# Optimization experiments

Hardware: AMD Instinct MI355X
Metric: run time of the kernel (lower is better)

The kernel has to match this reference:

```python
import math
import jax, jax.numpy as jnp
import numpy as np

B, S, D, H = 4, 1024, 1024, 16
DK = D // H
NEG = jnp.float32(-1e32)
EPS = 1e-5


def setup_inputs() -> dict:
    key = jax.random.key(0)
    ks = jax.random.split(key, 10)
    s = 1.0 / math.sqrt(D)
    return {
        "query": jax.random.normal(ks[0], (B, S, D), jnp.float32),
        "key": jax.random.normal(ks[1], (B, S, D), jnp.float32),
        "values": jax.random.normal(ks[2], (B, S, D), jnp.float32),
        "lens": jax.random.randint(ks[3], (B,), 0, S).astype(jnp.int32),
        "state_weight": jax.random.normal(ks[4], (1, H, S, S), jnp.float32),
        # params (kq_same=True -> k shares q_linear weights)
        "Wq": jax.random.normal(ks[5], (D, D), jnp.float32) * s,
        "bq": jnp.zeros((D,), jnp.float32),
        "Wv": jax.random.normal(ks[6], (D, D), jnp.float32) * s,
        "bv": jnp.zeros((D,), jnp.float32),
        "Wo": jax.random.normal(ks[7], (D, D), jnp.float32) * s,
        "bo": jnp.zeros((D,), jnp.float32),
        "gamma": jnp.ones((D,), jnp.float32),
        "beta": jnp.zeros((D,), jnp.float32),
    }


def reference(query, key, values, lens, state_weight, Wq, bq, Wv, bv, Wo, bo, gamma, beta):
    # eval-mode forward of DTransformerLayer (peek_cur=False -> strictly causal)
    b, s, d = query.shape
    mask = jnp.tril(jnp.ones((s, s), bool), -1)[None, None]  # [1,1,S,S]

    q = (query @ Wq + bq).reshape(b, s, H, DK).transpose(0, 2, 1, 3)   # bhsd
    k = (key @ Wq + bq).reshape(b, s, H, DK).transpose(0, 2, 1, 3)     # shared weights (kq_same)
    v = (values @ Wv + bv).reshape(b, s, H, DK).transpose(0, 2, 1, 3)

    scores = jnp.einsum('bhqd,bhkd->bhqk', q, k) / math.sqrt(DK)
    scores = jnp.where(mask, scores, NEG)
    scores = jnp.where(mask, scores + state_weight, NEG)
    attn = jax.nn.softmax(scores, axis=-1)
    attn = jnp.where(mask, attn, 0.0)  # fully-masked rows (row 0) -> zeros, matching torch

    ctx = jnp.einsum('bhqk,bhkd->bhqd', attn, v).transpose(0, 2, 1, 3).reshape(b, s, d)
    out = ctx @ Wo + bo

    x = query + out  # dropout is identity in eval
    mu = jnp.mean(x, axis=-1, keepdims=True)
    var = jnp.mean(jnp.square(x - mu), axis=-1, keepdims=True)
    return (x - mu) * jax.lax.rsqrt(var + EPS) * gamma + beta
```

## Files before the change

kernel.cpp:

```cpp
#include <hip/hip_runtime.h>

#define B_ 4
#define S_ 1024
#define D_ 1024
#define H_ 16
#define DK_ 64

typedef __attribute__((ext_vector_type(8))) short short8;
typedef __attribute__((ext_vector_type(4))) float f32x4;
typedef __attribute__((ext_vector_type(16))) float f32x16;

static __device__ __forceinline__ unsigned bf16rne(float x) {
    unsigned b = __float_as_uint(x);
    return (b + 0x7FFFu + ((b >> 16) & 1u)) >> 16;
}

__global__ __launch_bounds__(256) void cvt3_bf16(
    const float* __restrict__ q, const float* __restrict__ k,
    const float* __restrict__ v, ushort* __restrict__ out)
{
    const size_t i = ((size_t)blockIdx.x * 256 + threadIdx.x) * 8;
    const size_t FM = (size_t)4 * 1024 * 1024;
    const float* in = (i < FM) ? q : (i < 2 * FM) ? k : v;
    const size_t off = i & (FM - 1);
    const float4 a = *reinterpret_cast<const float4*>(in + off);
    const float4 b = *reinterpret_cast<const float4*>(in + off + 4);
    union { ushort u[8]; int4 vv; } p;
    p.u[0] = (ushort)bf16rne(a.x); p.u[1] = (ushort)bf16rne(a.y);
    p.u[2] = (ushort)bf16rne(a.z); p.u[3] = (ushort)bf16rne(a.w);
    p.u[4] = (ushort)bf16rne(b.x); p.u[5] = (ushort)bf16rne(b.y);
    p.u[6] = (ushort)bf16rne(b.z); p.u[7] = (ushort)bf16rne(b.w);
    *reinterpret_cast<int4*>(out + i) = p.vv;
}

__global__ __launch_bounds__(256) void transpose_cvt3(
    const float* __restrict__ W0, const float* __restrict__ W1,
    const float* __restrict__ W2, ushort* __restrict__ T0,
    ushort* __restrict__ T1, ushort* __restrict__ T2)
{
    __shared__ float ts[32][33];
    const float* W = (blockIdx.z == 0) ? W0 : (blockIdx.z == 1) ? W1 : W2;
    ushort*     Wt = (blockIdx.z == 0) ? T0 : (blockIdx.z == 1) ? T1 : T2;
    const int t  = threadIdx.x;
    const int k0 = blockIdx.y * 32, n0 = blockIdx.x * 32;
    const int r  = t >> 3, c4 = (t & 7) * 4;
    const float4 v = *reinterpret_cast<const float4*>(&W[(size_t)(k0 + r) * 1024 + n0 + c4]);
    ts[r][c4] = v.x; ts[r][c4 + 1] = v.y; ts[r][c4 + 2] = v.z; ts[r][c4 + 3] = v.w;
    __syncthreads();
    ushort4 o;
    o.x = (ushort)bf16rne(ts[c4    ][r]);
    o.y = (ushort)bf16rne(ts[c4 + 1][r]);
    o.z = (ushort)bf16rne(ts[c4 + 2][r]);
    o.w = (ushort)bf16rne(ts[c4 + 3][r]);
    *reinterpret_cast<ushort4*>(&Wt[(size_t)(n0 + r) * 1024 + k0 + c4]) = o;
}

template<int MODE>
__global__ __launch_bounds__(256) void gemm_mfma(
    const ushort* __restrict__ X, const ushort* __restrict__ Wt,
    const float* __restrict__ bias, const float* __restrict__ resid,
    void* __restrict__ out0, void* __restrict__ out1)
{
    __shared__ ushort As[64 * 64];
    __shared__ ushort Bs[128 * 64];

    const int t    = threadIdx.x;
    const int lane = t & 63;
    const int w    = t >> 6;

    const int cpx     = gridDim.x >> 3;
    const int logical = (blockIdx.x & 7) * cpx + (blockIdx.x >> 3);
    const int bm = logical >> 3;
    const int bn = logical & 7;

    const int srow   = lane >> 3;
    const int schunk = (lane & 7) ^ srow;
    const ushort* ag[2];
    const ushort* bg[4];
#pragma unroll
    for (int j = 0; j < 2; ++j)
        ag[j] = X  + (size_t)(bm * 64 + (j * 4 + w) * 8 + srow) * 1024 + schunk * 8;
#pragma unroll
    for (int j = 0; j < 4; ++j)
        bg[j] = Wt + (size_t)(bn * 128 + (j * 4 + w) * 8 + srow) * 1024 + schunk * 8;

#define STAGE(k0)                                                                \
    do {                                                                         \
        _Pragma("unroll")                                                        \
        for (int j = 0; j < 2; ++j)                                              \
            __builtin_amdgcn_global_load_lds(                                    \
                (__attribute__((address_space(1))) const void*)(ag[j] + (k0)),   \
                (__attribute__((address_space(3))) void*)&As[(j * 4 + w) * 512], \
                16, 0, 0);                                                       \
        _Pragma("unroll")                                                        \
        for (int j = 0; j < 4; ++j)                                              \
            __builtin_amdgcn_global_load_lds(                                    \
                (__attribute__((address_space(1))) const void*)(bg[j] + (k0)),   \
                (__attribute__((address_space(3))) void*)&Bs[(j * 4 + w) * 512], \
                16, 0, 0);                                                       \
    } while (0)

    const int fr = lane & 15;
    const int fk = lane >> 4;
    const int wm = w >> 1, wn = w & 1;

    f32x4 acc[2][4];
#pragma unroll
    for (int m = 0; m < 2; ++m)
#pragma unroll
        for (int n = 0; n < 4; ++n) acc[m][n] = (f32x4){0.f, 0.f, 0.f, 0.f};

#pragma unroll 1
    for (int kt = 0; kt < 16; ++kt) {
        STAGE(kt * 64);
        __syncthreads();
#pragma unroll
        for (int ks = 0; ks < 2; ++ks) {
            short8 af[2], bf[4];
#pragma unroll
            for (int m = 0; m < 2; ++m) {
                const int row = wm * 32 + m * 16 + fr;
                af[m] = *reinterpret_cast<const short8*>(
                    &As[row * 64 + (((ks * 4 + fk) ^ (row & 7)) * 8)]);
            }
#pragma unroll
            for (int n = 0; n < 4; ++n) {
                const int row = wn * 64 + n * 16 + fr;
                bf[n] = *reinterpret_cast<const short8*>(
                    &Bs[row * 64 + (((ks * 4 + fk) ^ (row & 7)) * 8)]);
            }
#pragma unroll
            for (int m = 0; m < 2; ++m)
#pragma unroll
                for (int n = 0; n < 4; ++n)
                    acc[m][n] = __builtin_amdgcn_mfma_f32_16x16x32_bf16(
                        af[m], bf[n], acc[m][n], 0, 0, 0);
        }
        __syncthreads();
    }
#undef STAGE

#pragma unroll
    for (int m = 0; m < 2; ++m) {
        const int row0 = bm * 64 + wm * 32 + m * 16 + fk * 4;
#pragma unroll
        for (int n = 0; n < 4; ++n) {
            const int col = bn * 128 + wn * 64 + n * 16 + fr;
            const float bc = bias[col];
            if (MODE == 0) {
                float* o = (float*)out0;
#pragma unroll
                for (int j = 0; j < 4; ++j) {
                    const int row = row0 + j;
                    o[(size_t)row * 1024 + col] =
                        acc[m][n][j] + bc + resid[(size_t)row * 1024 + col];
                }
            } else if (MODE == 1) {
                ushort* o = (row0 < 4096) ? (ushort*)out0 : (ushort*)out1;
                const int r0 = row0 & 4095;
                const int b_ = r0 >> 10, s0 = r0 & 1023;
                const int h  = col >> 6,  dk = col & 63;
#pragma unroll
                for (int j = 0; j < 4; ++j)
                    o[(((size_t)b_ * H_ + h) * S_ + s0 + j) * DK_ + dk] =
                        (ushort)bf16rne(acc[m][n][j] + bc);
            } else {
                ushort* o = (ushort*)out0;
                const int b_ = row0 >> 10, s0 = row0 & 1023;
                const int h  = col >> 6,   dk = col & 63;
                ushort4 pk;
                pk.x = (ushort)bf16rne(acc[m][n][0] + bc);
                pk.y = (ushort)bf16rne(acc[m][n][1] + bc);
                pk.z = (ushort)bf16rne(acc[m][n][2] + bc);
                pk.w = (ushort)bf16rne(acc[m][n][3] + bc);
                *reinterpret_cast<ushort4*>(
                    &o[(((size_t)b_ * H_ + h) * DK_ + dk) * S_ + s0]) = pk;
            }
        }
    }
}

__global__ __launch_bounds__(256) void attn_mfma(
    const ushort* __restrict__ Qh, const ushort* __restrict__ Kh,
    const ushort* __restrict__ Vt, const float* __restrict__ SW,
    ushort* __restrict__ ctx)
{
    __shared__ ushort Ks[2][64 * 64];
    __shared__ ushort Vs[2][64 * 64];

    const int t    = threadIdx.x;
    const int lane = t & 63;
    const int w    = t >> 6;
    const int bid  = blockIdx.x;
    const int bh   = bid & 63;
    const int b    = bh >> 4;
    const int h    = bh & 15;
    int qb = bid >> 6;
    qb = (qb < 4) ? qb : 11 - qb;

    const int ql = lane & 31;
    const int hi = lane >> 5;
    const int qrow  = qb * 128 + ql * 4 + w;
    const int maxt  = 2 * qb + 2;

    const ushort* Kg  = Kh + (size_t)bh * S_ * DK_;
    const ushort* Vg  = Vt + (size_t)bh * DK_ * S_;
    const float*  swp = SW + ((size_t)h * S_ + qrow) * S_;

    const int srow   = lane >> 3;
    const int schunk = (lane & 7) ^ srow;
    const ushort* kg[2];
    const ushort* vg[2];
#pragma unroll
    for (int j = 0; j < 2; ++j) {
        kg[j] = Kg + (size_t)((j * 4 + w) * 8 + srow) * DK_ + schunk * 8;
        vg[j] = Vg + (size_t)((j * 4 + w) * 8 + srow) * S_  + schunk * 8;
    }

#define ASTAGE(buf, k0)                                                          \
    do {                                                                         \
        _Pragma("unroll")                                                        \
        for (int j = 0; j < 2; ++j) {                                            \
            __builtin_amdgcn_global_load_lds(                                    \
                (__attribute__((address_space(1))) const void*)(kg[j] + (size_t)(k0) * DK_), \
                (__attribute__((address_space(3))) void*)&Ks[buf][(j * 4 + w) * 512], \
                16, 0, 0);                                                       \
            __builtin_amdgcn_global_load_lds(                                    \
                (__attribute__((address_space(1))) const void*)(vg[j] + (k0)),   \
                (__attribute__((address_space(3))) void*)&Vs[buf][(j * 4 + w) * 512], \
                16, 0, 0);                                                       \
        }                                                                        \
    } while (0)

    short8 qf[4];
    {
        const ushort* Qg = Qh + ((size_t)bh * S_ + qrow) * DK_;
#pragma unroll
        for (int c = 0; c < 4; ++c) {
            union { int4 i; short8 s; } u;
            u.i = *reinterpret_cast<const int4*>(&Qg[c * 16 + hi * 8]);
            qf[c] = u.s;
        }
    }

    f32x16 accA, accB;
#pragma unroll
    for (int r = 0; r < 16; ++r) { accA[r] = 0.f; accB[r] = 0.f; }
    float mrow = -1e30f, lrow = 0.f;

    ASTAGE(0, 0);

#pragma unroll 1
    for (int kt = 0; kt < maxt; ++kt) {
        const int cur = kt & 1;
        const int k0  = kt * 64;
        if (kt + 1 < maxt) {
            ASTAGE(cur ^ 1, (kt + 1) * 64);
            asm volatile("s_waitcnt vmcnt(4)" ::: "memory");
        } else {
            asm volatile("s_waitcnt vmcnt(0)" ::: "memory");
        }
        __builtin_amdgcn_s_barrier();
        __builtin_amdgcn_sched_barrier(0);

        f32x16 sc[2];
#pragma unroll
        for (int g = 0; g < 2; ++g) {
#pragma unroll
            for (int r = 0; r < 16; ++r) sc[g][r] = 0.f;
            const int row = g * 32 + ql;
#pragma unroll
            for (int c = 0; c < 4; ++c) {
                union { int2 p[2]; short8 s; } u;
                const int ch = ((c * 2 + hi) ^ (row & 7)) * 8;
                u.p[0] = *reinterpret_cast<const int2*>(&Ks[cur][row * 64 + ch]);
                u.p[1] = *reinterpret_cast<const int2*>(&Ks[cur][row * 64 + ch + 4]);
                sc[g] = __builtin_amdgcn_mfma_f32_32x32x16_bf16(u.s, qf[c], sc[g], 0, 0, 0);
            }
        }

        float swv[2][16];
#pragma unroll
        for (int g = 0; g < 2; ++g)
#pragma unroll
            for (int j = 0; j < 4; ++j) {
                const float4 v = *reinterpret_cast<const float4*>(
                    &swp[k0 + g * 32 + hi * 4 + j * 8]);
                swv[g][j * 4 + 0] = v.x; swv[g][j * 4 + 1] = v.y;
                swv[g][j * 4 + 2] = v.z; swv[g][j * 4 + 3] = v.w;
            }

        float p[2][16];
        float tmax = -1e30f;
#pragma unroll
        for (int g = 0; g < 2; ++g)
#pragma unroll
            for (int r = 0; r < 16; ++r) {
                const int key = k0 + g * 32 + (r & 3) + ((r >> 2) << 3) + (hi << 2);
                const float s = (key < qrow) ? sc[g][r] * 0.125f + swv[g][r] : -1e30f;
                p[g][r] = s;
                tmax = fmaxf(tmax, s);
            }
        tmax = fmaxf(tmax, __shfl_xor(tmax, 32, 64));
        const float mnew = fmaxf(mrow, tmax);
        const float corr = __expf(mrow - mnew);
        float psum = 0.f;
#pragma unroll
        for (int g = 0; g < 2; ++g)
#pragma unroll
            for (int r = 0; r < 16; ++r) {
                const float e = (p[g][r] > -1e29f) ? __expf(p[g][r] - mnew) : 0.f;
                p[g][r] = e;
                psum += e;
            }
        psum += __shfl_xor(psum, 32, 64);
        lrow = lrow * corr + psum;
        mrow = mnew;
#pragma unroll
        for (int r = 0; r < 16; ++r) { accA[r] *= corr; accB[r] *= corr; }

        short8 paf[4];
#pragma unroll
        for (int g = 0; g < 2; ++g) {
            unsigned pk[8];
#pragma unroll
            for (int j = 0; j < 8; ++j)
                pk[j] = bf16rne(p[g][2 * j]) | (bf16rne(p[g][2 * j + 1]) << 16);
            unsigned x0 = (unsigned)__shfl_xor((int)pk[0], 32, 64);
            unsigned x1 = (unsigned)__shfl_xor((int)pk[1], 32, 64);
            unsigned x2 = (unsigned)__shfl_xor((int)pk[2], 32, 64);
            unsigned x3 = (unsigned)__shfl_xor((int)pk[3], 32, 64);
            unsigned x4 = (unsigned)__shfl_xor((int)pk[4], 32, 64);
            unsigned x5 = (unsigned)__shfl_xor((int)pk[5], 32, 64);
            unsigned x6 = (unsigned)__shfl_xor((int)pk[6], 32, 64);
            unsigned x7 = (unsigned)__shfl_xor((int)pk[7], 32, 64);
            union { unsigned u[4]; short8 s; } a0, a1;
            a0.u[0] = hi ? x2 : pk[0];
            a0.u[1] = hi ? x3 : pk[1];
            a0.u[2] = hi ? pk[2] : x0;
            a0.u[3] = hi ? pk[3] : x1;
            a1.u[0] = hi ? x6 : pk[4];
            a1.u[1] = hi ? x7 : pk[5];
            a1.u[2] = hi ? pk[6] : x4;
            a1.u[3] = hi ? pk[7] : x5;
            paf[g * 2 + 0] = a0.s;
            paf[g * 2 + 1] = a1.s;
        }

#pragma unroll
        for (int cc = 0; cc < 4; ++cc) {
            const int rowA = ql, rowB = ql + 32;
            const int chA = ((cc * 2 + hi) ^ (rowA & 7)) * 8;
            union { int2 pp[2]; short8 s; } va, vb;
            va.pp[0] = *reinterpret_cast<const int2*>(&Vs[cur][rowA * 64 + chA]);
            va.pp[1] = *reinterpret_cast<const int2*>(&Vs[cur][rowA * 64 + chA + 4]);
            vb.pp[0] = *reinterpret_cast<const int2*>(&Vs[cur][rowB * 64 + chA]);
            vb.pp[1] = *reinterpret_cast<const int2*>(&Vs[cur][rowB * 64 + chA + 4]);
            accA = __builtin_amdgcn_mfma_f32_32x32x16_bf16(va.s, paf[cc], accA, 0, 0, 0);
            accB = __builtin_amdgcn_mfma_f32_32x32x16_bf16(vb.s, paf[cc], accB, 0, 0, 0);
        }

        __builtin_amdgcn_sched_barrier(0);
        __builtin_amdgcn_s_barrier();
        __builtin_amdgcn_sched_barrier(0);
    }
#undef ASTAGE

    const float inv = (lrow > 0.f) ? 1.f / lrow : 0.f;
    ushort* crow_ = ctx + ((size_t)b * S_ + qrow) * D_ + h * DK_;
#pragma unroll
    for (int g = 0; g < 4; ++g) {
        ushort4 oA, oB;
        oA.x = (ushort)bf16rne(accA[4 * g + 0] * inv);
        oA.y = (ushort)bf16rne(accA[4 * g + 1] * inv);
        oA.z = (ushort)bf16rne(accA[4 * g + 2] * inv);
        oA.w = (ushort)bf16rne(accA[4 * g + 3] * inv);
        oB.x = (ushort)bf16rne(accB[4 * g + 0] * inv);
        oB.y = (ushort)bf16rne(accB[4 * g + 1] * inv);
        oB.z = (ushort)bf16rne(accB[4 * g + 2] * inv);
        oB.w = (ushort)bf16rne(accB[4 * g + 3] * inv);
        *reinterpret_cast<ushort4*>(&crow_[g * 8 + hi * 4])      = oA;
        *reinterpret_cast<ushort4*>(&crow_[g * 8 + hi * 4 + 32]) = oB;
    }
}

__global__ __launch_bounds__(256) void layernorm_k(
    const float* __restrict__ x, const float* __restrict__ gamma,
    const float* __restrict__ beta, float* __restrict__ out)
{
    const int row = blockIdx.x;
    const int t   = threadIdx.x;
    const float4 v = *reinterpret_cast<const float4*>(&x[(size_t)row * D_ + (t << 2)]);
    float sum = v.x + v.y + v.z + v.w;
    float sq  = v.x * v.x + v.y * v.y + v.z * v.z + v.w * v.w;
#pragma unroll
    for (int w = 1; w < 64; w <<= 1) {
        sum += __shfl_xor(sum, w, 64);
        sq  += __shfl_xor(sq,  w, 64);
    }
    __shared__ float red[8];
    const int wid = t >> 6;
    if ((t & 63) == 0) { red[wid] = sum; red[wid + 4] = sq; }
    __syncthreads();
    sum = red[0] + red[1] + red[2] + red[3];
    sq  = red[4] + red[5] + red[6] + red[7];
    const float mu  = sum * (1.f / 1024.f);
    const float var = sq * (1.f / 1024.f) - mu * mu;
    const float rs  = rsqrtf(var + 1e-5f);
    const float4 gm = *reinterpret_cast<const float4*>(&gamma[t << 2]);
    const float4 bt = *reinterpret_cast<const float4*>(&beta[t << 2]);
    float4 o;
    o.x = (v.x - mu) * rs * gm.x + bt.x;
    o.y = (v.y - mu) * rs * gm.y + bt.y;
    o.z = (v.z - mu) * rs * gm.z + bt.z;
    o.w = (v.w - mu) * rs * gm.w + bt.w;
    *reinterpret_cast<float4*>(&out[(size_t)row * D_ + (t << 2)]) = o;
}

extern "C" void kernel_launch(void* const* d_in, const int* in_sizes, int n_in,
                              void* d_out, int out_size, void* d_ws, size_t ws_size,
                              hipStream_t stream)
{
    const float* query  = (const float*)d_in[0];
    const float* key    = (const float*)d_in[1];
    const float* values = (const float*)d_in[2];
    const float* SW     = (const float*)d_in[4];
    const float* Wq     = (const float*)d_in[5];
    const float* bq     = (const float*)d_in[6];
    const float* Wv     = (const float*)d_in[7];
    const float* bv     = (const float*)d_in[8];
    const float* Wo     = (const float*)d_in[9];
    const float* bo     = (const float*)d_in[10];
    const float* gamma  = (const float*)d_in[11];
    const float* beta   = (const float*)d_in[12];

    char* ws = (char*)d_ws;
    const size_t MB = 1024 * 1024;
    ushort* qbf = (ushort*)(ws);
    ushort* kbf = (ushort*)(ws +  8 * MB);
    ushort* vbf = (ushort*)(ws + 16 * MB);
    ushort* Wqt = (ushort*)(ws + 24 * MB);
    ushort* Wvt = (ushort*)(ws + 26 * MB);
    ushort* Wot = (ushort*)(ws + 28 * MB);
    ushort* Qh  = (ushort*)(ws + 30 * MB);
    ushort* Kh  = (ushort*)(ws + 38 * MB);
    ushort* Vt  = (ushort*)(ws + 46 * MB);
    ushort* ctxb = qbf;
    float*  xbf  = (float*)(ws + 8 * MB);

    const dim3 blk(256);

    cvt3_bf16<<<dim3(6144), blk, 0, stream>>>(query, key, values, qbf);
    transpose_cvt3<<<dim3(32, 32, 3), blk, 0, stream>>>(Wq, Wv, Wo, Wqt, Wvt, Wot);

    gemm_mfma<1><<<dim3(1024), blk, 0, stream>>>(qbf, Wqt, bq, nullptr, Qh, Kh);
    gemm_mfma<2><<<dim3(512),  blk, 0, stream>>>(vbf, Wvt, bv, nullptr, Vt, nullptr);

    attn_mfma<<<dim3(512), blk, 0, stream>>>(Qh, Kh, Vt, SW, ctxb);

    gemm_mfma<0><<<dim3(512), blk, 0, stream>>>(ctxb, Wot, bo, query, xbf, nullptr);

    layernorm_k<<<dim3(4096), blk, 0, stream>>>(xbf, gamma, beta, (float*)d_out);
}
```

Measured before the change: 139.6 us.

## Split attention key range into two partitions with flash-decoding style merge

Each query block's key tiles are split into two halves, each processed by its own workgroup, doubling the attention grid to 1024 blocks. Partial contexts are written in bf16 along with per-row running max and sum, and a new merge kernel combines them with softmax rescaling. The K/V tiles in shared memory are also relaid out so each lane reads a contiguous 16-byte fragment instead of two swizzled 8-byte reads. This adds an extra kernel launch, extra global traffic for the partials, and an extra bf16 rounding step in exchange for better CU occupancy across the causal workload.

```diff
diff --git a/kernel.cpp b/kernel.cpp
--- a/kernel.cpp
+++ b/kernel.cpp
@@ -183,10 +183,10 @@
 __global__ __launch_bounds__(256) void attn_mfma(
     const ushort* __restrict__ Qh, const ushort* __restrict__ Kh,
     const ushort* __restrict__ Vt, const float* __restrict__ SW,
-    ushort* __restrict__ ctx)
-{
-    __shared__ ushort Ks[2][64 * 64];
-    __shared__ ushort Vs[2][64 * 64];
+    ushort* __restrict__ ctxP, float2* __restrict__ ml)
+{
+    __shared__ ushort Ks[2][4096];
+    __shared__ ushort Vs[2][4096];
 
     const int t    = threadIdx.x;
     const int lane = t & 63;
@@ -195,39 +195,43 @@
     const int bh   = bid & 63;
     const int b    = bh >> 4;
     const int h    = bh & 15;
-    int qb = bid >> 6;
+    const int qp   = bid >> 6;
+    const int p    = qp >> 3;
+    int qb = qp & 7;
     qb = (qb < 4) ? qb : 11 - qb;
 
     const int ql = lane & 31;
     const int hi = lane >> 5;
-    const int qrow  = qb * 128 + ql * 4 + w;
-    const int maxt  = 2 * qb + 2;
+    const int qrow = qb * 128 + ql * 4 + w;
+    const int t0 = p * (qb + 1);
+    const int nt = qb + 1;
 
     const ushort* Kg  = Kh + (size_t)bh * S_ * DK_;
     const ushort* Vg  = Vt + (size_t)bh * DK_ * S_;
     const float*  swp = SW + ((size_t)h * S_ + qrow) * S_;
 
-    const int srow   = lane >> 3;
-    const int schunk = (lane & 7) ^ srow;
-    const ushort* kg[2];
-    const ushort* vg[2];
+    const ushort* kgp[2];
+    const ushort* vgp[2];
 #pragma unroll
     for (int j = 0; j < 2; ++j) {
-        kg[j] = Kg + (size_t)((j * 4 + w) * 8 + srow) * DK_ + schunk * 8;
-        vg[j] = Vg + (size_t)((j * 4 + w) * 8 + srow) * S_  + schunk * 8;
+        const int bb = w * 2 + j;
+        const int g = bb >> 2, c = bb & 3;
+        kgp[j] = Kg + (size_t)(g * 32 + ql) * DK_ + c * 16 + hi * 8;
+        vgp[j] = Vg + (size_t)(g * 32 + ql) * S_  + c * 16 + hi * 8;
     }
 
 #define ASTAGE(buf, k0)                                                          \
     do {                                                                         \
         _Pragma("unroll")                                                        \
         for (int j = 0; j < 2; ++j) {                                            \
+            const int bb = w * 2 + j;                                            \
             __builtin_amdgcn_global_load_lds(                                    \
-                (__attribute__((address_space(1))) const void*)(kg[j] + (size_t)(k0) * DK_), \
-                (__attribute__((address_space(3))) void*)&Ks[buf][(j * 4 + w) * 512], \
+                (__attribute__((address_space(1))) const void*)(kgp[j] + (size_t)(k0) * DK_), \
+                (__attribute__((address_space(3))) void*)&Ks[buf][bb * 512],     \
                 16, 0, 0);                                                       \
             __builtin_amdgcn_global_load_lds(                                    \
-                (__attribute__((address_space(1))) const void*)(vg[j] + (k0)),   \
-                (__attribute__((address_space(3))) void*)&Vs[buf][(j * 4 + w) * 512], \
+                (__attribute__((address_space(1))) const void*)(vgp[j] + (k0)),  \
+                (__attribute__((address_space(3))) void*)&Vs[buf][bb * 512],     \
                 16, 0, 0);                                                       \
         }                                                                        \
     } while (0)
@@ -248,14 +252,14 @@
     for (int r = 0; r < 16; ++r) { accA[r] = 0.f; accB[r] = 0.f; }
     float mrow = -1e30f, lrow = 0.f;
 
-    ASTAGE(0, 0);
+    ASTAGE(0, t0 * 64);
 
 #pragma unroll 1
-    for (int kt = 0; kt < maxt; ++kt) {
+    for (int kt = 0; kt < nt; ++kt) {
         const int cur = kt & 1;
-        const int k0  = kt * 64;
-        if (kt + 1 < maxt) {
-            ASTAGE(cur ^ 1, (kt + 1) * 64);
+        const int k0  = (t0 + kt) * 64;
+        if (kt + 1 < nt) {
+            ASTAGE(cur ^ 1, (t0 + kt + 1) * 64);
             asm volatile("s_waitcnt vmcnt(4)" ::: "memory");
         } else {
             asm volatile("s_waitcnt vmcnt(0)" ::: "memory");
@@ -268,14 +272,11 @@
         for (int g = 0; g < 2; ++g) {
 #pragma unroll
             for (int r = 0; r < 16; ++r) sc[g][r] = 0.f;
-            const int row = g * 32 + ql;
 #pragma unroll
             for (int c = 0; c < 4; ++c) {
-                union { int2 p[2]; short8 s; } u;
-                const int ch = ((c * 2 + hi) ^ (row & 7)) * 8;
-                u.p[0] = *reinterpret_cast<const int2*>(&Ks[cur][row * 64 + ch]);
-                u.p[1] = *reinterpret_cast<const int2*>(&Ks[cur][row * 64 + ch + 4]);
-                sc[g] = __builtin_amdgcn_mfma_f32_32x32x16_bf16(u.s, qf[c], sc[g], 0, 0, 0);
+                const short8 kf = *reinterpret_cast<const short8*>(
+                    &Ks[cur][((g * 4 + c) * 64 + lane) * 8]);
+                sc[g] = __builtin_amdgcn_mfma_f32_32x32x16_bf16(kf, qf[c], sc[g], 0, 0, 0);
             }
         }
 
@@ -290,7 +291,7 @@
                 swv[g][j * 4 + 2] = v.z; swv[g][j * 4 + 3] = v.w;
             }
 
-        float p[2][16];
+        float pr[2][16];
         float tmax = -1e30f;
 #pragma unroll
         for (int g = 0; g < 2; ++g)
@@ -298,7 +299,7 @@
             for (int r = 0; r < 16; ++r) {
                 const int key = k0 + g * 32 + (r & 3) + ((r >> 2) << 3) + (hi << 2);
                 const float s = (key < qrow) ? sc[g][r] * 0.125f + swv[g][r] : -1e30f;
-                p[g][r] = s;
+                pr[g][r] = s;
                 tmax = fmaxf(tmax, s);
             }
         tmax = fmaxf(tmax, __shfl_xor(tmax, 32, 64));
@@ -309,8 +310,8 @@
         for (int g = 0; g < 2; ++g)
 #pragma unroll
             for (int r = 0; r < 16; ++r) {
-                const float e = (p[g][r] > -1e29f) ? __expf(p[g][r] - mnew) : 0.f;
-                p[g][r] = e;
+                const float e = (pr[g][r] > -1e29f) ? __expf(pr[g][r] - mnew) : 0.f;
+                pr[g][r] = e;
                 psum += e;
             }
         psum += __shfl_xor(psum, 32, 64);
@@ -325,7 +326,7 @@
             unsigned pk[8];
 #pragma unroll
             for (int j = 0; j < 8; ++j)
-                pk[j] = bf16rne(p[g][2 * j]) | (bf16rne(p[g][2 * j + 1]) << 16);
+                pk[j] = bf16rne(pr[g][2 * j]) | (bf16rne(pr[g][2 * j + 1]) << 16);
             unsigned x0 = (unsigned)__shfl_xor((int)pk[0], 32, 64);
             unsigned x1 = (unsigned)__shfl_xor((int)pk[1], 32, 64);
             unsigned x2 = (unsigned)__shfl_xor((int)pk[2], 32, 64);
@@ -349,15 +350,12 @@
 
 #pragma unroll
         for (int cc = 0; cc < 4; ++cc) {
-            const int rowA = ql, rowB = ql + 32;
-            const int chA = ((cc * 2 + hi) ^ (rowA & 7)) * 8;
-            union { int2 pp[2]; short8 s; } va, vb;
-            va.pp[0] = *reinterpret_cast<const int2*>(&Vs[cur][rowA * 64 + chA]);
-            va.pp[1] = *reinterpret_cast<const int2*>(&Vs[cur][rowA * 64 + chA + 4]);
-            vb.pp[0] = *reinterpret_cast<const int2*>(&Vs[cur][rowB * 64 + chA]);
-            vb.pp[1] = *reinterpret_cast<const int2*>(&Vs[cur][rowB * 64 + chA + 4]);
-            accA = __builtin_amdgcn_mfma_f32_32x32x16_bf16(va.s, paf[cc], accA, 0, 0, 0);
-            accB = __builtin_amdgcn_mfma_f32_32x32x16_bf16(vb.s, paf[cc], accB, 0, 0, 0);
+            const short8 va = *reinterpret_cast<const short8*>(
+                &Vs[cur][((0 * 4 + cc) * 64 + lane) * 8]);
+            const short8 vb = *reinterpret_cast<const short8*>(
+                &Vs[cur][((1 * 4 + cc) * 64 + lane) * 8]);
+            accA = __builtin_amdgcn_mfma_f32_32x32x16_bf16(va, paf[cc], accA, 0, 0, 0);
+            accB = __builtin_amdgcn_mfma_f32_32x32x16_bf16(vb, paf[cc], accB, 0, 0, 0);
         }
 
         __builtin_amdgcn_sched_barrier(0);
@@ -367,7 +365,8 @@
 #undef ASTAGE
 
     const float inv = (lrow > 0.f) ? 1.f / lrow : 0.f;
-    ushort* crow_ = ctx + ((size_t)b * S_ + qrow) * D_ + h * DK_;
+    ushort* crow_ = ctxP + (size_t)p * 4194304 +
+                    ((size_t)b * S_ + qrow) * D_ + h * DK_;
 #pragma unroll
     for (int g = 0; g < 4; ++g) {
         ushort4 oA, oB;
@@ -382,6 +381,40 @@
         *reinterpret_cast<ushort4*>(&crow_[g * 8 + hi * 4])      = oA;
         *reinterpret_cast<ushort4*>(&crow_[g * 8 + hi * 4 + 32]) = oB;
     }
+    if (hi == 0) {
+        float2 v; v.x = mrow; v.y = lrow;
+        ml[((size_t)p * 64 + bh) * 1024 + qrow] = v;
+    }
+}
+
+__global__ __launch_bounds__(256) void attn_merge(
+    const ushort* __restrict__ ctxP, const float2* __restrict__ ml,
+    ushort* __restrict__ ctx)
+{
+    const size_t idx = ((size_t)blockIdx.x * 256 + threadIdx.x) * 8;
+    const int col = (int)(idx & 1023);
+    const int row = (int)(idx >> 10);
+    const int b = row >> 10, s = row & 1023;
+    const int h = col >> 6;
+    const int bh = b * 16 + h;
+    const float2 ml0 = ml[(size_t)bh * 1024 + s];
+    const float2 ml1 = ml[(size_t)(64 + bh) * 1024 + s];
+    const float m  = fmaxf(ml0.x, ml1.x);
+    const float a0 = ml0.y * __expf(ml0.x - m);
+    const float a1 = ml1.y * __expf(ml1.x - m);
+    const float d  = a0 + a1;
+    const float w0 = (d > 0.f) ? a0 / d : 0.f;
+    const float w1 = (d > 0.f) ? a1 / d : 0.f;
+    union { int4 v; ushort u[8]; } p0, p1, o;
+    p0.v = *reinterpret_cast<const int4*>(ctxP + idx);
+    p1.v = *reinterpret_cast<const int4*>(ctxP + 4194304 + idx);
+#pragma unroll
+    for (int i = 0; i < 8; ++i) {
+        const float f0 = __uint_as_float((unsigned)p0.u[i] << 16);
+        const float f1 = __uint_as_float((unsigned)p1.u[i] << 16);
+        o.u[i] = (ushort)bf16rne(w0 * f0 + w1 * f1);
+    }
+    *reinterpret_cast<int4*>(ctx + idx) = o.v;
 }
 
 __global__ __launch_bounds__(256) void layernorm_k(
@@ -436,17 +469,19 @@
 
     char* ws = (char*)d_ws;
     const size_t MB = 1024 * 1024;
-    ushort* qbf = (ushort*)(ws);
-    ushort* kbf = (ushort*)(ws +  8 * MB);
-    ushort* vbf = (ushort*)(ws + 16 * MB);
-    ushort* Wqt = (ushort*)(ws + 24 * MB);
-    ushort* Wvt = (ushort*)(ws + 26 * MB);
-    ushort* Wot = (ushort*)(ws + 28 * MB);
-    ushort* Qh  = (ushort*)(ws + 30 * MB);
-    ushort* Kh  = (ushort*)(ws + 38 * MB);
-    ushort* Vt  = (ushort*)(ws + 46 * MB);
-    ushort* ctxb = qbf;
-    float*  xbf  = (float*)(ws + 8 * MB);
+    ushort* qbf  = (ushort*)(ws);
+    ushort* kbf  = (ushort*)(ws +  8 * MB);
+    ushort* vbf  = (ushort*)(ws + 16 * MB);
+    ushort* Wqt  = (ushort*)(ws + 24 * MB);
+    ushort* Wvt  = (ushort*)(ws + 26 * MB);
+    ushort* Wot  = (ushort*)(ws + 28 * MB);
+    ushort* Qh   = (ushort*)(ws + 30 * MB);
+    ushort* Kh   = (ushort*)(ws + 38 * MB);
+    ushort* Vt   = (ushort*)(ws + 46 * MB);
+    float2* ml   = (float2*)(ws + 54 * MB);
+    ushort* ctxP = qbf;
+    ushort* ctxm = vbf;
+    float*  xbf  = (float*)(ws + 30 * MB);
 
     const dim3 blk(256);
 
@@ -456,9 +491,10 @@
     gemm_mfma<1><<<dim3(1024), blk, 0, stream>>>(qbf, Wqt, bq, nullptr, Qh, Kh);
     gemm_mfma<2><<<dim3(512),  blk, 0, stream>>>(vbf, Wvt, bv, nullptr, Vt, nullptr);
 
-    attn_mfma<<<dim3(512), blk, 0, stream>>>(Qh, Kh, Vt, SW, ctxb);
-
-    gemm_mfma<0><<<dim3(512), blk, 0, stream>>>(ctxb, Wot, bo, query, xbf, nullptr);
+    attn_mfma<<<dim3(1024), blk, 0, stream>>>(Qh, Kh, Vt, SW, ctxP, ml);
+    attn_merge<<<dim3(2048), blk, 0, stream>>>(ctxP, ml, ctxm);
+
+    gemm_mfma<0><<<dim3(512), blk, 0, stream>>>(ctxm, Wot, bo, query, xbf, nullptr);
 
     layernorm_k<<<dim3(4096), blk, 0, stream>>>(xbf, gamma, beta, (float*)d_out);
 }
```

After: 144.2 us. +3.2%, slower.
